# Optimization experiments

Hardware: AMD Instinct MI355X
Metric: run time of the kernel (lower is better)

Reference implementation:

```python
import jax, jax.numpy as jnp
import numpy as np

N_CLASS = 12
N_OVO = N_CLASS * (N_CLASS - 1) // 2  # 66
_I_IDX, _J_IDX = np.triu_indices(N_CLASS, k=1)  # static pair -> (winner_if_pos, winner_if_neg)


def _resize_bilinear(x, size):
    # torch F.interpolate(mode='bilinear', align_corners=False) == jax half-pixel bilinear
    return jax.image.resize(x, (x.shape[0], x.shape[1], size, size), method='bilinear')


def _vote(o):
    # o: [N, n_ovo, H, W] pairwise logits -> [N, n_class, H, W] vote counts
    v = (o > 0).astype(o.dtype)                 # 1 where class i beats class j
    vt = jnp.swapaxes(v, 0, 1)                  # [P, N, H, W], pair axis leading
    res = (jax.ops.segment_sum(vt, jnp.asarray(_I_IDX), num_segments=N_CLASS)
           + jax.ops.segment_sum(1.0 - vt, jnp.asarray(_J_IDX), num_segments=N_CLASS))
    return jnp.swapaxes(res, 0, 1)              # [N, n_class, H, W]


def setup_inputs() -> dict:
    key = jax.random.key(0)
    ks = jax.random.split(key, 12)
    dims = [512, 256, 128, 64]
    sizes = [32, 64, 128, 256]
    N = 8
    inp = {}
    for i, (d, s) in enumerate(zip(dims, sizes)):
        inp[f"stage{i}"] = jax.random.normal(ks[i], (N, d, s, s), dtype=jnp.float32)
        inp[f"w{i}"] = jax.random.normal(ks[4 + i], (N_OVO, d), dtype=jnp.float32) * 0.05
        inp[f"b{i}"] = jax.random.normal(ks[8 + i], (N_OVO,), dtype=jnp.float32) * 0.05
    inp["last_only"] = 1
    return inp


def reference(stage0, stage1, stage2, stage3, w0, w1, w2, w3, b0, b1, b2, b3, last_only):
    stages = [stage0, stage1, stage2, stage3]
    ws = [w0, w1, w2, w3]
    bs = [b0, b1, b2, b3]
    # 1x1 convs: [N,C,H,W] x [O,C] -> [N,O,H,W]
    outputs = [jnp.einsum('nchw,oc->nohw', s, w) + b[None, :, None, None]
               for s, w, b in zip(stages, ws, bs)]
    if last_only:
        size = stages[-1].shape[2]
        total = outputs[0] * 0  # placeholder shape via sum below
        layers = [_resize_bilinear(o, size) for o in outputs]
        acc = layers[0]
        for l in layers[1:]:
            acc = acc + l
        outputs = [acc]
    else:
        for i in range(1, len(stages)):
            size = stages[i].shape[2]
            acc = outputs[i]
            for o in outputs[:i]:
                acc = acc + _resize_bilinear(o, size)
            outputs.append(acc)
    voted = tuple(_vote(o) for o in outputs)
    return voted[0] if last_only else voted
```

## Files before the change

kernel.cpp:

```cpp
#include <hip/hip_runtime.h>
#include <cstdint>
#include <cstddef>


#define N_BATCH 8
#define N_OVO   66
#define N_CLS   12

__constant__ unsigned char PAIR_I[N_OVO] = {
  0,0,0,0,0,0,0,0,0,0,0,
  1,1,1,1,1,1,1,1,1,1,
  2,2,2,2,2,2,2,2,2,
  3,3,3,3,3,3,3,3,
  4,4,4,4,4,4,4,
  5,5,5,5,5,5,
  6,6,6,6,6,
  7,7,7,7,
  8,8,8,
  9,9,
  10
};
__constant__ unsigned char PAIR_J[N_OVO] = {
  1,2,3,4,5,6,7,8,9,10,11,
  2,3,4,5,6,7,8,9,10,11,
  3,4,5,6,7,8,9,10,11,
  4,5,6,7,8,9,10,11,
  5,6,7,8,9,10,11,
  6,7,8,9,10,11,
  7,8,9,10,11,
  8,9,10,11,
  9,10,11,
  10,11,
  11
};

__device__ float W3T[64 * N_OVO];

template<int C, int S2, int OG>
__device__ __forceinline__
void conv_body(int b, const float* __restrict__ x, const float* __restrict__ w,
               const float* __restrict__ bias, float* __restrict__ out)
{
    constexpr int NOG = N_OVO / OG;
    constexpr int PX  = S2 / 256;
    const int og  = b % NOG;
    int rest      = b / NOG;
    const int pxb = rest % PX;
    const int n   = rest / PX;
    const int o0  = og * OG;
    const int p   = pxb * 256 + threadIdx.x;

    float acc[OG];
#pragma unroll
    for (int oi = 0; oi < OG; ++oi) acc[oi] = 0.0f;

    const float* xb = x + (size_t)n * C * S2 + p;
    for (int c0 = 0; c0 < C; c0 += 8) {
        float xr[8];
#pragma unroll
        for (int k = 0; k < 8; ++k)
            xr[k] = xb[(size_t)(c0 + k) * S2];
#pragma unroll
        for (int oi = 0; oi < OG; ++oi) {
            const float* wrow = w + (size_t)(o0 + oi) * C + c0;
#pragma unroll
            for (int k = 0; k < 8; ++k)
                acc[oi] = __fmaf_rn(wrow[k], xr[k], acc[oi]);
        }
    }

    float* op = out + ((size_t)n * S2 + p) * N_OVO + o0;
#pragma unroll
    for (int oi = 0; oi < OG; ++oi)
        op[oi] = __fadd_rn(acc[oi], bias[o0 + oi]);
}

#define B0 192
#define B1 768
#define B2 3072

__global__ __launch_bounds__(256)
void conv_all(const float* __restrict__ x0, const float* __restrict__ w0,
              const float* __restrict__ b0, float* __restrict__ c0,
              const float* __restrict__ x1, const float* __restrict__ w1,
              const float* __restrict__ b1, float* __restrict__ c1,
              const float* __restrict__ x2, const float* __restrict__ w2,
              const float* __restrict__ b2, float* __restrict__ c2,
              const float* __restrict__ w3)
{
    const int bid = blockIdx.x;
    if (bid < B0) {
        conv_body<512, 1024, 11>(bid, x0, w0, b0, c0);
    } else if (bid < B0 + B1) {
        conv_body<256, 4096, 11>(bid - B0, x1, w1, b1, c1);
    } else if (bid < B0 + B1 + B2) {
        conv_body<128, 16384, 11>(bid - (B0 + B1), x2, w2, b2, c2);
    } else {
        for (int idx = threadIdx.x; idx < 64 * N_OVO; idx += 256) {
            int c = idx / N_OVO; int o = idx - c * N_OVO;
            W3T[idx] = w3[o * 64 + c];
        }
    }
}

#define WT0 4
#define WT1 6
#define WT2 10


template<int WT, int SS>
__device__ __forceinline__ void stage_tile(float* __restrict__ t,
                                           const float* __restrict__ src,
                                           int y0, int x0)
{
    constexpr int RELS = WT * WT;
    for (int idx = threadIdx.x; idx < RELS * 33; idx += 256) {
        int r  = idx / 33;
        int k  = idx - r * 33;
        int ry = r / WT, rx = r - ry * WT;
        int sy = min(max(y0 + ry, 0), SS - 1);
        int sx = min(max(x0 + rx, 0), SS - 1);
        const float2 v = *reinterpret_cast<const float2*>(
            src + ((size_t)sy * SS + sx) * N_OVO + 2 * k);
        int dst;
        if (k < 32) {
            int sr = r ^ ((r >> 3) & 3);
            dst = ((k >> 1) * RELS + sr) * 4 + (k & 1) * 2;
        } else {
            dst = 64 * RELS + r * 2;
        }
        *reinterpret_cast<float2*>(t + dst) = v;
    }
}

__device__ __forceinline__ float bil1(float v00, float v01, float v10, float v11,
                                      float wy, float wy0, float wx, float wx0,
                                      int ysing, int xsing)
{
    float u0 = ysing ? v00 : __fmaf_rn(wy, v10, __fmul_rn(wy0, v00));
    float u1 = ysing ? v01 : __fmaf_rn(wy, v11, __fmul_rn(wy0, v01));
    return xsing ? u0 : __fmaf_rn(wx, u1, __fmul_rn(wx0, u0));
}

template<int RELS>
__device__ __forceinline__ float4 bil4(const float* __restrict__ t, int g,
                                       int s00, int s01, int s10, int s11,
                                       float wy, float wx, int ysing, int xsing)
{
    const float* base = t + g * (RELS * 4);
    float4 v00 = *reinterpret_cast<const float4*>(base + s00 * 4);
    float4 v01 = *reinterpret_cast<const float4*>(base + s01 * 4);
    float4 v10 = *reinterpret_cast<const float4*>(base + s10 * 4);
    float4 v11 = *reinterpret_cast<const float4*>(base + s11 * 4);
    float wy0 = 1.0f - wy, wx0 = 1.0f - wx;
    float4 r;
    r.x = bil1(v00.x, v01.x, v10.x, v11.x, wy, wy0, wx, wx0, ysing, xsing);
    r.y = bil1(v00.y, v01.y, v10.y, v11.y, wy, wy0, wx, wx0, ysing, xsing);
    r.z = bil1(v00.z, v01.z, v10.z, v11.z, wy, wy0, wx, wx0, ysing, xsing);
    r.w = bil1(v00.w, v01.w, v10.w, v11.w, wy, wy0, wx, wx0, ysing, xsing);
    return r;
}

__global__ __launch_bounds__(256, 3)
void fuse_vote(const float* __restrict__ x3,
               const float* __restrict__ b3,
               const float* __restrict__ c0buf, const float* __restrict__ c1buf,
               const float* __restrict__ c2buf,
               float* __restrict__ out)
{
    const int n  = blockIdx.z;
    const int tx = threadIdx.x & 15, ty = threadIdx.x >> 4;
    const int X0 = blockIdx.x * 16,  Y0 = blockIdx.y * 16;
    const int X  = X0 + tx,          Y  = Y0 + ty;

    __shared__ alignas(16) float t0s[16  * N_OVO];
    __shared__ alignas(16) float t1s[36  * N_OVO];
    __shared__ alignas(16) float t2s[100 * N_OVO];

    int rel00[3], rel01[3], rel10[3], rel11[3], ysing[3], xsing[3];
    int s00[3], s01[3], s10[3], s11[3];
    float wxv[3], wyv[3];
    int x0raw[3], y0raw[3];
    const int   Ss[3]   = {32, 64, 128};
    const float invs[3] = {32.0f / 256.0f, 64.0f / 256.0f, 128.0f / 256.0f};
    const int   Wt[3]   = {WT0, WT1, WT2};
#pragma unroll
    for (int s = 0; s < 3; ++s) {
        float inv = invs[s];
        int S = Ss[s];
        x0raw[s] = (int)floorf(((float)X0 + 0.5f) * inv - 0.5f);
        y0raw[s] = (int)floorf(((float)Y0 + 0.5f) * inv - 0.5f);
        float fx = ((float)X + 0.5f) * inv - 0.5f;
        float fy = ((float)Y + 0.5f) * inv - 0.5f;
        int ix0 = (int)floorf(fx), iy0 = (int)floorf(fy);
        wxv[s] = fx - (float)ix0;  wyv[s] = fy - (float)iy0;
        xsing[s] = (ix0 < 0) || (ix0 + 1 > S - 1);
        ysing[s] = (iy0 < 0) || (iy0 + 1 > S - 1);
        int rx = ix0 - x0raw[s], ry = iy0 - y0raw[s];
        rel00[s] = ry * Wt[s] + rx;
        rel01[s] = rel00[s] + 1;
        rel10[s] = rel00[s] + Wt[s];
        rel11[s] = rel10[s] + 1;
        s00[s] = rel00[s] ^ ((rel00[s] >> 3) & 3);
        s01[s] = rel01[s] ^ ((rel01[s] >> 3) & 3);
        s10[s] = rel10[s] ^ ((rel10[s] >> 3) & 3);
        s11[s] = rel11[s] ^ ((rel11[s] >> 3) & 3);
    }

    stage_tile<WT0, 32 >(t0s, c0buf + (size_t)n * 1024  * N_OVO, y0raw[0], x0raw[0]);
    stage_tile<WT1, 64 >(t1s, c1buf + (size_t)n * 4096  * N_OVO, y0raw[1], x0raw[1]);
    stage_tile<WT2, 128>(t2s, c2buf + (size_t)n * 16384 * N_OVO, y0raw[2], x0raw[2]);

    float acc[N_OVO];
#pragma unroll
    for (int o = 0; o < N_OVO; ++o) acc[o] = 0.0f;

    {
        const float* xp = x3 + (size_t)n * 64 * 65536 + (size_t)Y * 256 + X;
#pragma unroll 4
        for (int c = 0; c < 64; ++c) {
            float xv = xp[(size_t)c * 65536];
            const float* wc = W3T + c * N_OVO;
#pragma unroll
            for (int o = 0; o < N_OVO; ++o)
                acc[o] = __fmaf_rn(wc[o], xv, acc[o]);
        }
    }

    __syncthreads();

    unsigned long long packed = 0;

#pragma unroll
    for (int g = 0; g < 16; ++g) {
        const int o = g * 4;
        float4 L3;
        L3.x = __fadd_rn(acc[o],     b3[o]);
        L3.y = __fadd_rn(acc[o + 1], b3[o + 1]);
        L3.z = __fadd_rn(acc[o + 2], b3[o + 2]);
        L3.w = __fadd_rn(acc[o + 3], b3[o + 3]);

        float4 s0 = bil4<16 >(t0s, g, s00[0], s01[0], s10[0], s11[0],
                              wyv[0], wxv[0], ysing[0], xsing[0]);
        float4 s1 = bil4<36 >(t1s, g, s00[1], s01[1], s10[1], s11[1],
                              wyv[1], wxv[1], ysing[1], xsing[1]);
        float4 s2 = bil4<100>(t2s, g, s00[2], s01[2], s10[2], s11[2],
                              wyv[2], wxv[2], ysing[2], xsing[2]);

        float v0 = __fadd_rn(__fadd_rn(__fadd_rn(s0.x, s1.x), s2.x), L3.x);
        float v1 = __fadd_rn(__fadd_rn(__fadd_rn(s0.y, s1.y), s2.y), L3.y);
        float v2 = __fadd_rn(__fadd_rn(__fadd_rn(s0.z, s1.z), s2.z), L3.z);
        float v3 = __fadd_rn(__fadd_rn(__fadd_rn(s0.w, s1.w), s2.w), L3.w);

        packed += (v0 > 0.0f) ? (1ull << (4 * (int)PAIR_I[o]))
                              : (1ull << (4 * (int)PAIR_J[o]));
        packed += (v1 > 0.0f) ? (1ull << (4 * (int)PAIR_I[o + 1]))
                              : (1ull << (4 * (int)PAIR_J[o + 1]));
        packed += (v2 > 0.0f) ? (1ull << (4 * (int)PAIR_I[o + 2]))
                              : (1ull << (4 * (int)PAIR_J[o + 2]));
        packed += (v3 > 0.0f) ? (1ull << (4 * (int)PAIR_I[o + 3]))
                              : (1ull << (4 * (int)PAIR_J[o + 3]));
    }

    {
        float L3a = __fadd_rn(acc[64], b3[64]);
        float L3b = __fadd_rn(acc[65], b3[65]);

        float La[3], Lb[3];
#pragma unroll
        for (int s = 0; s < 3; ++s) {
            const float* t = (s == 0) ? t0s : (s == 1) ? t1s : t2s;
            const int RELS = Wt[s] * Wt[s];
            const float* tb = t + 64 * RELS;
            float2 v00 = *reinterpret_cast<const float2*>(tb + rel00[s] * 2);
            float2 v01 = *reinterpret_cast<const float2*>(tb + rel01[s] * 2);
            float2 v10 = *reinterpret_cast<const float2*>(tb + rel10[s] * 2);
            float2 v11 = *reinterpret_cast<const float2*>(tb + rel11[s] * 2);
            float wy = wyv[s], wx = wxv[s];
            float wy0 = 1.0f - wy, wx0 = 1.0f - wx;
            La[s] = bil1(v00.x, v01.x, v10.x, v11.x, wy, wy0, wx, wx0, ysing[s], xsing[s]);
            Lb[s] = bil1(v00.y, v01.y, v10.y, v11.y, wy, wy0, wx, wx0, ysing[s], xsing[s]);
        }
        float ta = __fadd_rn(__fadd_rn(__fadd_rn(La[0], La[1]), La[2]), L3a);
        float tb = __fadd_rn(__fadd_rn(__fadd_rn(Lb[0], Lb[1]), Lb[2]), L3b);
        packed += (ta > 0.0f) ? (1ull << (4 * (int)PAIR_I[64]))
                              : (1ull << (4 * (int)PAIR_J[64]));
        packed += (tb > 0.0f) ? (1ull << (4 * (int)PAIR_I[65]))
                              : (1ull << (4 * (int)PAIR_J[65]));
    }

    float* op = out + (size_t)n * N_CLS * 65536 + (size_t)Y * 256 + X;
#pragma unroll
    for (int k = 0; k < N_CLS; ++k)
        op[(size_t)k * 65536] = (float)(int)((packed >> (4 * k)) & 15ull);
}

extern "C" void kernel_launch(void* const* d_in, const int* in_sizes, int n_in,
                              void* d_out, int out_size, void* d_ws, size_t ws_size,
                              hipStream_t stream)
{
    const float* stage0 = (const float*)d_in[0];
    const float* w0     = (const float*)d_in[1];
    const float* b0     = (const float*)d_in[2];
    const float* stage1 = (const float*)d_in[3];
    const float* w1     = (const float*)d_in[4];
    const float* b1     = (const float*)d_in[5];
    const float* stage2 = (const float*)d_in[6];
    const float* w2     = (const float*)d_in[7];
    const float* b2     = (const float*)d_in[8];
    const float* stage3 = (const float*)d_in[9];
    const float* w3     = (const float*)d_in[10];
    const float* b3     = (const float*)d_in[11];
    float* out = (float*)d_out;

    float* c0 = (float*)d_ws;
    float* c1 = c0 + (size_t)540672;
    float* c2 = c1 + (size_t)2162688;

    conv_all<<<dim3(B0 + B1 + B2 + 1), 256, 0, stream>>>(
        stage0, w0, b0, c0,
        stage1, w1, b1, c1,
        stage2, w2, b2, c2,
        w3);

    fuse_vote<<<dim3(16, 16, N_BATCH), 256, 0, stream>>>(stage3, b3, c0, c1, c2, out);
}
```

Baseline: 478.2 us.

## Stage w3 transposed in LDS per block and preload stage3 channels into registers

```diff
diff --git a/kernel.cpp b/kernel.cpp
--- a/kernel.cpp
+++ b/kernel.cpp
@@ -34,8 +34,6 @@
   11
 };
 
-__device__ float W3T[64 * N_OVO];
-
 template<int C, int S2, int OG>
 __device__ __forceinline__
 void conv_body(int b, const float* __restrict__ x, const float* __restrict__ w,
@@ -85,27 +83,22 @@
               const float* __restrict__ x1, const float* __restrict__ w1,
               const float* __restrict__ b1, float* __restrict__ c1,
               const float* __restrict__ x2, const float* __restrict__ w2,
-              const float* __restrict__ b2, float* __restrict__ c2,
-              const float* __restrict__ w3)
+              const float* __restrict__ b2, float* __restrict__ c2)
 {
     const int bid = blockIdx.x;
     if (bid < B0) {
         conv_body<512, 1024, 11>(bid, x0, w0, b0, c0);
     } else if (bid < B0 + B1) {
         conv_body<256, 4096, 11>(bid - B0, x1, w1, b1, c1);
-    } else if (bid < B0 + B1 + B2) {
+    } else {
         conv_body<128, 16384, 11>(bid - (B0 + B1), x2, w2, b2, c2);
-    } else {
-        for (int idx = threadIdx.x; idx < 64 * N_OVO; idx += 256) {
-            int c = idx / N_OVO; int o = idx - c * N_OVO;
-            W3T[idx] = w3[o * 64 + c];
-        }
     }
 }
 
 #define WT0 4
 #define WT1 6
 #define WT2 10
+#define WROW 68
 
 
 template<int WT, int SS>
@@ -161,8 +154,8 @@
     return r;
 }
 
-__global__ __launch_bounds__(256, 3)
-void fuse_vote(const float* __restrict__ x3,
+__global__ __launch_bounds__(256, 2)
+void fuse_vote(const float* __restrict__ x3, const float* __restrict__ w3,
                const float* __restrict__ b3,
                const float* __restrict__ c0buf, const float* __restrict__ c1buf,
                const float* __restrict__ c2buf,
@@ -176,6 +169,7 @@
     __shared__ alignas(16) float t0s[16  * N_OVO];
     __shared__ alignas(16) float t1s[36  * N_OVO];
     __shared__ alignas(16) float t2s[100 * N_OVO];
+    __shared__ alignas(16) float wlds[64 * WROW];
 
     int rel00[3], rel01[3], rel10[3], rel11[3], ysing[3], xsing[3];
     int s00[3], s01[3], s10[3], s11[3];
@@ -207,27 +201,41 @@
         s11[s] = rel11[s] ^ ((rel11[s] >> 3) & 3);
     }
 
+    for (int idx = threadIdx.x; idx < 64 * N_OVO; idx += 256) {
+        int o = idx >> 6, c = idx & 63;
+        wlds[c * WROW + o] = w3[idx];
+    }
+
     stage_tile<WT0, 32 >(t0s, c0buf + (size_t)n * 1024  * N_OVO, y0raw[0], x0raw[0]);
     stage_tile<WT1, 64 >(t1s, c1buf + (size_t)n * 4096  * N_OVO, y0raw[1], x0raw[1]);
     stage_tile<WT2, 128>(t2s, c2buf + (size_t)n * 16384 * N_OVO, y0raw[2], x0raw[2]);
 
-    float acc[N_OVO];
-#pragma unroll
-    for (int o = 0; o < N_OVO; ++o) acc[o] = 0.0f;
-
+    float xr[64];
     {
         const float* xp = x3 + (size_t)n * 64 * 65536 + (size_t)Y * 256 + X;
-#pragma unroll 4
-        for (int c = 0; c < 64; ++c) {
-            float xv = xp[(size_t)c * 65536];
-            const float* wc = W3T + c * N_OVO;
-#pragma unroll
-            for (int o = 0; o < N_OVO; ++o)
-                acc[o] = __fmaf_rn(wc[o], xv, acc[o]);
-        }
+#pragma unroll
+        for (int c = 0; c < 64; ++c) xr[c] = xp[(size_t)c * 65536];
     }
 
     __syncthreads();
+
+    float acc[N_OVO];
+#pragma unroll
+    for (int o = 0; o < N_OVO; ++o) acc[o] = 0.0f;
+
+#pragma unroll 1
+    for (int c = 0; c < 64; ++c) {
+        const float* wrow = &wlds[c * WROW];
+        float wv[68];
+#pragma unroll
+        for (int q = 0; q < 17; ++q)
+            *reinterpret_cast<float4*>(&wv[4 * q]) =
+                *reinterpret_cast<const float4*>(wrow + 4 * q);
+        float xv = xr[c];
+#pragma unroll
+        for (int o = 0; o < N_OVO; ++o)
+            acc[o] = __fmaf_rn(wv[o], xv, acc[o]);
+    }
 
     unsigned long long packed = 0;
 
@@ -317,11 +325,10 @@
     float* c1 = c0 + (size_t)540672;
     float* c2 = c1 + (size_t)2162688;
 
-    conv_all<<<dim3(B0 + B1 + B2 + 1), 256, 0, stream>>>(
+    conv_all<<<dim3(B0 + B1 + B2), 256, 0, stream>>>(
         stage0, w0, b0, c0,
         stage1, w1, b1, c1,
-        stage2, w2, b2, c2,
-        w3);
-
-    fuse_vote<<<dim3(16, 16, N_BATCH), 256, 0, stream>>>(stage3, b3, c0, c1, c2, out);
-}
+        stage2, w2, b2, c2);
+
+    fuse_vote<<<dim3(16, 16, N_BATCH), 256, 0, stream>>>(stage3, w3, b3, c0, c1, c2, out);
+}
```

Result: slower. 567.6 us (+18.7%).
